# Kernel optimization log

Measured on AMD Instinct MI355X. Metric: run time of the kernel, lower is better.

The kernel has to match this reference:

```python
import jax, jax.numpy as jnp
import numpy as np

NUM_LEVELS = 3
NUM_EMBEDDINGS = 1024
EMBEDDING_DIM = 128
COMMITMENT_COST = 0.25
N_TOKENS = 262144


def setup_inputs() -> dict:
    key = jax.random.key(0)
    k1, k2 = jax.random.split(key)
    z_e = jax.random.normal(k1, (N_TOKENS, EMBEDDING_DIM), dtype=jnp.float32)
    codebooks = jax.random.normal(k2, (NUM_LEVELS, NUM_EMBEDDINGS, EMBEDDING_DIM), dtype=jnp.float32)
    return {"z_e": z_e, "codebooks": codebooks}


def _rvq_forward(z_e, codebooks):
    """Sequential residual VQ: per level cdist + argmin + gather + residual update.

    Per-level losses follow the standard EMA-VQ formulation:
      vq_loss     = mean((z_q - sg(residual))^2)
      commit_loss = beta * mean((sg(z_q) - residual)^2)
    with straight-through estimator z_q_st = residual + sg(z_q - residual).
    """
    sg = jax.lax.stop_gradient
    residual = z_e
    z_q_total = jnp.zeros_like(z_e)
    all_indices = []
    vq_loss = jnp.float32(0.0)
    commit_loss = jnp.float32(0.0)
    num_levels = codebooks.shape[0]
    for lvl in range(num_levels):  # small fixed loop over levels (sequential by design)
        E = codebooks[lvl]  # [K, D]
        # squared-distance matrix [N, K]: ||r||^2 + ||e||^2 - 2 r.e
        d = (jnp.sum(residual * residual, axis=1, keepdims=True)
             + jnp.sum(E * E, axis=1)
             - 2.0 * (residual @ E.T))
        idx = jnp.argmin(d, axis=1)           # [N]
        z_q = E[idx]                           # gather [N, D]
        vq_loss = vq_loss + jnp.mean((z_q - sg(residual)) ** 2)
        commit_loss = commit_loss + COMMITMENT_COST * jnp.mean((sg(z_q) - residual) ** 2)
        z_q_st = residual + sg(z_q - residual)  # straight-through
        z_q_total = z_q_total + z_q_st
        residual = residual - z_q_st
        all_indices.append(idx)
    L = jnp.float32(num_levels)
    stacked_indices = jnp.stack(all_indices, axis=1)  # [N, num_levels]
    return z_q_total, vq_loss / L, commit_loss / L, stacked_indices


def reference(z_e, codebooks):
    return _rvq_forward(z_e, codebooks)
```

## Files before the change

kernel.cpp:

```cpp
#include <hip/hip_runtime.h>
#include <math.h>

#define N_TOK   262144
#define DIMV    128
#define KCODE   1024
#define LEV     3
#define BLOCK   256
#define NTILES  64
#define EPS     0.08f

typedef _Float16 f16x8 __attribute__((ext_vector_type(8)));
typedef float f32x4 __attribute__((ext_vector_type(4)));


__global__ void rvq_prep(const float* __restrict__ cb, double* __restrict__ ws) {
    int c = blockIdx.x * blockDim.x + threadIdx.x;
    if (c == 0) ws[0] = 0.0;
    if (c < LEV * KCODE) {
        const float* e = cb + (size_t)c * DIMV;
        double s = 0.0;
        #pragma unroll 8
        for (int j = 0; j < DIMV; ++j) { double v = (double)e[j]; s = fma(v, v, s); }
        ws[8 + c] = s;
        ((float*)(ws + 8 + LEV * KCODE))[c] = (float)(s + 8192.0);
    }
}

__device__ inline void stage_write(unsigned char* dst, int woff, float4 g0, float4 g1) {
    f16x8 v;
    v[0]=(_Float16)g0.x; v[1]=(_Float16)g0.y; v[2]=(_Float16)g0.z; v[3]=(_Float16)g0.w;
    v[4]=(_Float16)g1.x; v[5]=(_Float16)g1.y; v[6]=(_Float16)g1.z; v[7]=(_Float16)g1.w;
    *(f16x8*)(dst + woff) = v;
}

__device__ inline unsigned sel4(const unsigned v[4], int j) {
    unsigned a = (j & 1) ? v[1] : v[0];
    unsigned b = (j & 1) ? v[3] : v[2];
    return (j & 2) ? b : a;
}

__global__ __launch_bounds__(BLOCK, 2) void rvq_main(const float* __restrict__ ze,
                                                     const float* __restrict__ cb,
                                                     float* __restrict__ out,
                                                     double* __restrict__ ws) {
    __shared__ __align__(16) unsigned char Bbuf[8][4096];
    __shared__ __align__(16) float eeS[KCODE];
    __shared__ double ssum[4];

    const double* __restrict__ ee64g = ws + 8;
    const float*  __restrict__ eebg  = (const float*)(ws + 8 + LEV * KCODE);

    const int tid  = threadIdx.x;
    const int lane = tid & 63;
    const int wid  = tid >> 6;
    const int q    = lane >> 4;
    const int col  = lane & 15;
    const long tokbase = (long)blockIdx.x * 128 + wid * 32;

    const int wc   = (((tid >> 2) & 3) << 6) | ((tid & 3) << 4) | (tid >> 4);
    const int woff = (wc ^ ((wc >> 4) & 7)) << 4;
    const int ro_e = (lane ^ (lane >> 4)) << 4;
    const int ro_o = (lane ^ 4 ^ (lane >> 4)) << 4;

    float r[2][4][8];
    f16x8 Ah[2][4], Al[2][4];

    #pragma unroll
    for (int mt = 0; mt < 2; ++mt) {
        const float4* zp = (const float4*)(ze + (size_t)(tokbase + mt*16 + col) * DIMV);
        #pragma unroll
        for (int st = 0; st < 4; ++st) {
            float4 a = zp[st*8 + q*2], b = zp[st*8 + q*2 + 1];
            r[mt][st][0]=a.x; r[mt][st][1]=a.y; r[mt][st][2]=a.z; r[mt][st][3]=a.w;
            r[mt][st][4]=b.x; r[mt][st][5]=b.y; r[mt][st][6]=b.z; r[mt][st][7]=b.w;
        }
    }
    #pragma unroll
    for (int mt = 0; mt < 2; ++mt)
        #pragma unroll
        for (int st = 0; st < 4; ++st) {
            f16x8 h, lo;
            #pragma unroll
            for (int j = 0; j < 8; ++j) {
                float y = -2.0f * r[mt][st][j];
                _Float16 hh = (_Float16)y;
                h[j] = hh;
                lo[j] = (_Float16)(y - (float)hh);
            }
            Ah[mt][st] = h; Al[mt][st] = lo;
        }

    double loss = 0.0;
    float* out_idx = out + (size_t)N_TOK * DIMV + 2;

    for (int l = 0; l < LEV; ++l) {
        __syncthreads();
        ((float4*)eeS)[tid] = ((const float4*)(eebg + (size_t)l * KCODE))[tid];
        {
            const float4* p = (const float4*)(cb + ((size_t)l*KCODE + (tid>>4)) * DIMV + (tid&15)*8);
            #pragma unroll
            for (int i = 0; i < 4; ++i) {
                stage_write(Bbuf[i], woff, p[0], p[1]);
                p += 512;
            }
        }
        __syncthreads();

        const float4* pp = (const float4*)(cb + ((size_t)l*KCODE + 64 + (tid>>4)) * DIMV + (tid&15)*8);

        unsigned m1[2][4], m2[2][4];
        #pragma unroll
        for (int mt = 0; mt < 2; ++mt)
            #pragma unroll
            for (int i = 0; i < 4; ++i) { m1[mt][i] = 0xFFFFFFFFu; m2[mt][i] = 0xFFFFFFFFu; }

        for (int tb = 0; tb < NTILES; tb += 4) {
            const int pre = (tb + 4 < NTILES);
            #pragma unroll
            for (int s = 0; s < 4; ++s) {
                const int t = tb + s;
                float4 g0, g1;
                if (pre) { g0 = pp[0]; g1 = pp[1]; pp += 512; }
                {
                    const unsigned char* bb = Bbuf[t & 7];
                    f16x8 B0 = *(const f16x8*)(bb + ro_e);
                    f16x8 B1 = *(const f16x8*)(bb + 1024 + ro_o);
                    f16x8 B2 = *(const f16x8*)(bb + 2048 + ro_e);
                    f16x8 B3 = *(const f16x8*)(bb + 3072 + ro_o);
                    float eeq = eeS[t*16 + col];
                    f32x4 c0  = {eeq, eeq, eeq, eeq};
                    f32x4 c1v = {eeq, eeq, eeq, eeq};
                    c0  = __builtin_amdgcn_mfma_f32_16x16x32_f16(Ah[0][0], B0, c0, 0,0,0);
                    c1v = __builtin_amdgcn_mfma_f32_16x16x32_f16(Ah[1][0], B0, c1v, 0,0,0);
                    c0  = __builtin_amdgcn_mfma_f32_16x16x32_f16(Al[0][0], B0, c0, 0,0,0);
                    c1v = __builtin_amdgcn_mfma_f32_16x16x32_f16(Al[1][0], B0, c1v, 0,0,0);
                    c0  = __builtin_amdgcn_mfma_f32_16x16x32_f16(Ah[0][1], B1, c0, 0,0,0);
                    c1v = __builtin_amdgcn_mfma_f32_16x16x32_f16(Ah[1][1], B1, c1v, 0,0,0);
                    c0  = __builtin_amdgcn_mfma_f32_16x16x32_f16(Al[0][1], B1, c0, 0,0,0);
                    c1v = __builtin_amdgcn_mfma_f32_16x16x32_f16(Al[1][1], B1, c1v, 0,0,0);
                    c0  = __builtin_amdgcn_mfma_f32_16x16x32_f16(Ah[0][2], B2, c0, 0,0,0);
                    c1v = __builtin_amdgcn_mfma_f32_16x16x32_f16(Ah[1][2], B2, c1v, 0,0,0);
                    c0  = __builtin_amdgcn_mfma_f32_16x16x32_f16(Al[0][2], B2, c0, 0,0,0);
                    c1v = __builtin_amdgcn_mfma_f32_16x16x32_f16(Al[1][2], B2, c1v, 0,0,0);
                    c0  = __builtin_amdgcn_mfma_f32_16x16x32_f16(Ah[0][3], B3, c0, 0,0,0);
                    c1v = __builtin_amdgcn_mfma_f32_16x16x32_f16(Ah[1][3], B3, c1v, 0,0,0);
                    c0  = __builtin_amdgcn_mfma_f32_16x16x32_f16(Al[0][3], B3, c0, 0,0,0);
                    c1v = __builtin_amdgcn_mfma_f32_16x16x32_f16(Al[1][3], B3, c1v, 0,0,0);
                    #pragma unroll
                    for (int i = 0; i < 4; ++i) {
                        unsigned k0 = (__float_as_uint(c0[i]) << 6) | (unsigned)t;
                        m2[0][i] = min(m2[0][i], max(m1[0][i], k0));
                        m1[0][i] = min(m1[0][i], k0);
                        unsigned k1_ = (__float_as_uint(c1v[i]) << 6) | (unsigned)t;
                        m2[1][i] = min(m2[1][i], max(m1[1][i], k1_));
                        m1[1][i] = min(m1[1][i], k1_);
                    }
                }
                if (pre) stage_write(Bbuf[(t+4)&7], woff, g0, g1);
            }
            __syncthreads();
        }

        unsigned k1[2][4], k2[2][4], q1[2][4], q2[2][4];
        #pragma unroll
        for (int mt = 0; mt < 2; ++mt)
            #pragma unroll
            for (int i = 0; i < 4; ++i) {
                k1[mt][i] = m1[mt][i]; k2[mt][i] = m2[mt][i];
                q1[mt][i] = (unsigned)col; q2[mt][i] = (unsigned)col;
            }
        #pragma unroll
        for (int d = 1; d <= 8; d <<= 1) {
            #pragma unroll
            for (int mt = 0; mt < 2; ++mt)
                #pragma unroll
                for (int i = 0; i < 4; ++i) {
                    unsigned ok1 = __shfl_xor(k1[mt][i], d), oq1 = __shfl_xor(q1[mt][i], d);
                    unsigned ok2 = __shfl_xor(k2[mt][i], d), oq2 = __shfl_xor(q2[mt][i], d);
                    bool sw = (ok1 < k1[mt][i]) || (ok1 == k1[mt][i] && oq1 < q1[mt][i]);
                    unsigned n1 = sw ? ok1 : k1[mt][i], nq1 = sw ? oq1 : q1[mt][i];
                    unsigned hk = sw ? k1[mt][i] : ok1, hq = sw ? q1[mt][i] : oq1;
                    bool s2 = (ok2 < k2[mt][i]) || (ok2 == k2[mt][i] && oq2 < q2[mt][i]);
                    unsigned p2 = s2 ? ok2 : k2[mt][i], pq = s2 ? oq2 : q2[mt][i];
                    bool s3 = (p2 < hk) || (p2 == hk && pq < hq);
                    k1[mt][i] = n1;              q1[mt][i] = nq1;
                    k2[mt][i] = s3 ? p2 : hk;    q2[mt][i] = s3 ? pq : hq;
                }
        }

        int jsel = (lane >> 2) & 3;
        int S = ((col >> 2) << 4) | ((col & 3) << 2);

        #pragma unroll
        for (int mt = 0; mt < 2; ++mt) {
            unsigned sk1 = sel4(k1[mt], jsel), sq1 = sel4(q1[mt], jsel);
            unsigned sk2 = sel4(k2[mt], jsel), sq2 = sel4(q2[mt], jsel);
            unsigned bk1 = (unsigned)__shfl((int)sk1, S);
            unsigned bq1 = (unsigned)__shfl((int)sq1, S);
            unsigned bk2 = (unsigned)__shfl((int)sk2, S);
            unsigned bq2 = (unsigned)__shfl((int)sq2, S);
            int c1c = (int)(((bk1 & 63u) << 4) | bq1);
            int c2c = (int)(((bk2 & 63u) << 4) | bq2);
            float d1 = __uint_as_float((bk1 >> 6) | 0x44000000u) - 8192.0f;
            float d2 = __uint_as_float((bk2 >> 6) | 0x44000000u) - 8192.0f;
            int bc = c1c;
            if (d2 - d1 < EPS) {
                double s1 = 0.0, s2d = 0.0;
                const float4* e1 = (const float4*)(cb + ((size_t)l*KCODE + c1c)*DIMV);
                const float4* e2 = (const float4*)(cb + ((size_t)l*KCODE + c2c)*DIMV);
                #pragma unroll
                for (int st = 0; st < 4; ++st) {
                    float4 a = e1[st*8 + q*2], b = e1[st*8 + q*2 + 1];
                    s1 = fma((double)a.x,(double)r[mt][st][0],s1); s1 = fma((double)a.y,(double)r[mt][st][1],s1);
                    s1 = fma((double)a.z,(double)r[mt][st][2],s1); s1 = fma((double)a.w,(double)r[mt][st][3],s1);
                    s1 = fma((double)b.x,(double)r[mt][st][4],s1); s1 = fma((double)b.y,(double)r[mt][st][5],s1);
                    s1 = fma((double)b.z,(double)r[mt][st][6],s1); s1 = fma((double)b.w,(double)r[mt][st][7],s1);
                    float4 a2 = e2[st*8 + q*2], b2 = e2[st*8 + q*2 + 1];
                    s2d = fma((double)a2.x,(double)r[mt][st][0],s2d); s2d = fma((double)a2.y,(double)r[mt][st][1],s2d);
                    s2d = fma((double)a2.z,(double)r[mt][st][2],s2d); s2d = fma((double)a2.w,(double)r[mt][st][3],s2d);
                    s2d = fma((double)b2.x,(double)r[mt][st][4],s2d); s2d = fma((double)b2.y,(double)r[mt][st][5],s2d);
                    s2d = fma((double)b2.z,(double)r[mt][st][6],s2d); s2d = fma((double)b2.w,(double)r[mt][st][7],s2d);
                }
                s1  += __shfl_xor(s1, 16);  s1  += __shfl_xor(s1, 32);
                s2d += __shfl_xor(s2d, 16); s2d += __shfl_xor(s2d, 32);
                double dd1 = ee64g[l*KCODE + c1c] - 2.0*s1;
                double dd2 = ee64g[l*KCODE + c2c] - 2.0*s2d;
                if (dd2 < dd1 || (dd2 == dd1 && c2c < c1c)) bc = c2c;
            }
            const float4* eb = (const float4*)(cb + ((size_t)l*KCODE + bc)*DIMV);
            #pragma unroll
            for (int st = 0; st < 4; ++st) {
                float4 a = eb[st*8 + q*2], b = eb[st*8 + q*2 + 1];
                float qv[8] = {a.x,a.y,a.z,a.w,b.x,b.y,b.z,b.w};
                #pragma unroll
                for (int j = 0; j < 8; ++j) {
                    float rv = r[mt][st][j];
                    float t1 = qv[j] - rv;
                    loss += (double)t1 * (double)t1;
                    float zqst = rv + t1;
                    r[mt][st][j] = rv - zqst;
                }
            }
            if (l < LEV - 1) {
                #pragma unroll
                for (int st = 0; st < 4; ++st) {
                    f16x8 h, lo;
                    #pragma unroll
                    for (int j = 0; j < 8; ++j) {
                        float y = -2.0f * r[mt][st][j];
                        _Float16 hh = (_Float16)y;
                        h[j] = hh;
                        lo[j] = (_Float16)(y - (float)hh);
                    }
                    Ah[mt][st] = h; Al[mt][st] = lo;
                }
            } else {
                const float4* zp = (const float4*)(ze + (size_t)(tokbase + mt*16 + col)*DIMV);
                float4* op = (float4*)(out + (size_t)(tokbase + mt*16 + col)*DIMV);
                #pragma unroll
                for (int st = 0; st < 4; ++st) {
                    float4 za = zp[st*8 + q*2], zb = zp[st*8 + q*2 + 1];
                    float4 oa, ob;
                    oa.x = za.x - r[mt][st][0]; oa.y = za.y - r[mt][st][1];
                    oa.z = za.z - r[mt][st][2]; oa.w = za.w - r[mt][st][3];
                    ob.x = zb.x - r[mt][st][4]; ob.y = zb.y - r[mt][st][5];
                    ob.z = zb.z - r[mt][st][6]; ob.w = zb.w - r[mt][st][7];
                    op[st*8 + q*2] = oa; op[st*8 + q*2 + 1] = ob;
                }
            }
            if (q == 0) out_idx[(size_t)(tokbase + mt*16 + col)*3 + l] = (float)bc;
        }
    }

    #pragma unroll
    for (int d = 1; d <= 32; d <<= 1) loss += __shfl_xor(loss, d);
    if ((tid & 63) == 0) ssum[wid] = loss;
    __syncthreads();
    if (tid == 0) atomicAdd(ws, ssum[0] + ssum[1] + ssum[2] + ssum[3]);
}

__global__ void rvq_fin(const double* __restrict__ ws, float* __restrict__ out) {
    double vq = ws[0] / ((double)N_TOK * (double)DIMV * (double)LEV);
    out[(size_t)N_TOK * DIMV + 0] = (float)vq;
    out[(size_t)N_TOK * DIMV + 1] = (float)(0.25 * vq);
}

extern "C" void kernel_launch(void* const* d_in, const int* in_sizes, int n_in,
                              void* d_out, int out_size, void* d_ws, size_t ws_size,
                              hipStream_t stream) {
    const float* ze = (const float*)d_in[0];
    const float* cb = (const float*)d_in[1];
    float* out = (float*)d_out;
    double* ws = (double*)d_ws;

    rvq_prep<<<(LEV * KCODE + 255) / 256, 256, 0, stream>>>(cb, ws);
    rvq_main<<<N_TOK / 128, BLOCK, 0, stream>>>(ze, cb, out, ws);
    rvq_fin<<<1, 1, 0, stream>>>(ws, out);
}
```

Baseline: 708.4 us.

## Prepack codebook into MFMA fragment layout and stream B operands from global

The prep kernel now converts each codebook to fp16 and writes it in the exact per-lane MFMA B-fragment layout in the workspace, alongside the norms. The main kernel drops shared-memory staging, the fp32-to-fp16 conversion and per-tile __syncthreads. Each wave instead loads its B fragments straight from global/L2 with a two-tile register double buffer. This removes LDS traffic and barriers but makes every wave read the codebook separately from cache, so the loop is more exposed to global load latency.

```diff
diff --git a/kernel.cpp b/kernel.cpp
--- a/kernel.cpp
+++ b/kernel.cpp
@@ -9,28 +9,38 @@
 #define NTILES  64
 #define EPS     0.08f
 
+#define WS_EE64_B  64
+#define WS_EE32_B  24640
+#define WS_FRAG_B  36928
+
 typedef _Float16 f16x8 __attribute__((ext_vector_type(8)));
 typedef float f32x4 __attribute__((ext_vector_type(4)));
-
 
 __global__ void rvq_prep(const float* __restrict__ cb, double* __restrict__ ws) {
     int c = blockIdx.x * blockDim.x + threadIdx.x;
     if (c == 0) ws[0] = 0.0;
-    if (c < LEV * KCODE) {
-        const float* e = cb + (size_t)c * DIMV;
-        double s = 0.0;
-        #pragma unroll 8
-        for (int j = 0; j < DIMV; ++j) { double v = (double)e[j]; s = fma(v, v, s); }
-        ws[8 + c] = s;
-        ((float*)(ws + 8 + LEV * KCODE))[c] = (float)(s + 8192.0);
-    }
-}
-
-__device__ inline void stage_write(unsigned char* dst, int woff, float4 g0, float4 g1) {
-    f16x8 v;
-    v[0]=(_Float16)g0.x; v[1]=(_Float16)g0.y; v[2]=(_Float16)g0.z; v[3]=(_Float16)g0.w;
-    v[4]=(_Float16)g1.x; v[5]=(_Float16)g1.y; v[6]=(_Float16)g1.z; v[7]=(_Float16)g1.w;
-    *(f16x8*)(dst + woff) = v;
+    if (c >= LEV * KCODE) return;
+    const float* e = cb + (size_t)c * DIMV;
+    const int lvl = c >> 10, ci = c & 1023, t4 = ci >> 4, n = ci & 15;
+    unsigned char* fb = (unsigned char*)ws + WS_FRAG_B + (((size_t)(lvl * 64 + t4)) << 12);
+    double s = 0.0;
+    #pragma unroll
+    for (int st = 0; st < 4; ++st)
+        #pragma unroll
+        for (int kq = 0; kq < 4; ++kq) {
+            float4 a = *(const float4*)(e + st*32 + kq*8);
+            float4 b = *(const float4*)(e + st*32 + kq*8 + 4);
+            f16x8 h;
+            h[0]=(_Float16)a.x; h[1]=(_Float16)a.y; h[2]=(_Float16)a.z; h[3]=(_Float16)a.w;
+            h[4]=(_Float16)b.x; h[5]=(_Float16)b.y; h[6]=(_Float16)b.z; h[7]=(_Float16)b.w;
+            s = fma((double)a.x,(double)a.x,s); s = fma((double)a.y,(double)a.y,s);
+            s = fma((double)a.z,(double)a.z,s); s = fma((double)a.w,(double)a.w,s);
+            s = fma((double)b.x,(double)b.x,s); s = fma((double)b.y,(double)b.y,s);
+            s = fma((double)b.z,(double)b.z,s); s = fma((double)b.w,(double)b.w,s);
+            *(f16x8*)(fb + st*1024 + ((kq*16 + n) << 4)) = h;
+        }
+    ((double*)((unsigned char*)ws + WS_EE64_B))[c] = s;
+    ((float*)((unsigned char*)ws + WS_EE32_B))[c] = (float)(s + 8192.0);
 }
 
 __device__ inline unsigned sel4(const unsigned v[4], int j) {
@@ -43,12 +53,11 @@
                                                      const float* __restrict__ cb,
                                                      float* __restrict__ out,
                                                      double* __restrict__ ws) {
-    __shared__ __align__(16) unsigned char Bbuf[8][4096];
-    __shared__ __align__(16) float eeS[KCODE];
     __shared__ double ssum[4];
 
-    const double* __restrict__ ee64g = ws + 8;
-    const float*  __restrict__ eebg  = (const float*)(ws + 8 + LEV * KCODE);
+    const double* __restrict__ ee64g = (const double*)((const unsigned char*)ws + WS_EE64_B);
+    const float*  __restrict__ eebg  = (const float*)((const unsigned char*)ws + WS_EE32_B);
+    const unsigned char* __restrict__ fbase = (const unsigned char*)ws + WS_FRAG_B;
 
     const int tid  = threadIdx.x;
     const int lane = tid & 63;
@@ -57,11 +66,6 @@
     const int col  = lane & 15;
     const long tokbase = (long)blockIdx.x * 128 + wid * 32;
 
-    const int wc   = (((tid >> 2) & 3) << 6) | ((tid & 3) << 4) | (tid >> 4);
-    const int woff = (wc ^ ((wc >> 4) & 7)) << 4;
-    const int ro_e = (lane ^ (lane >> 4)) << 4;
-    const int ro_o = (lane ^ 4 ^ (lane >> 4)) << 4;
-
     float r[2][4][8];
     f16x8 Ah[2][4], Al[2][4];
 
@@ -93,20 +97,45 @@
     double loss = 0.0;
     float* out_idx = out + (size_t)N_TOK * DIMV + 2;
 
+#define TILE_COMPUTE(B, EEQ, T)                                                      \
+    do {                                                                             \
+        f32x4 c0  = {(EEQ),(EEQ),(EEQ),(EEQ)};                                       \
+        f32x4 c1v = {(EEQ),(EEQ),(EEQ),(EEQ)};                                       \
+        c0  = __builtin_amdgcn_mfma_f32_16x16x32_f16(Ah[0][0], (B)[0], c0,  0,0,0);  \
+        c1v = __builtin_amdgcn_mfma_f32_16x16x32_f16(Ah[1][0], (B)[0], c1v, 0,0,0);  \
+        c0  = __builtin_amdgcn_mfma_f32_16x16x32_f16(Al[0][0], (B)[0], c0,  0,0,0);  \
+        c1v = __builtin_amdgcn_mfma_f32_16x16x32_f16(Al[1][0], (B)[0], c1v, 0,0,0);  \
+        c0  = __builtin_amdgcn_mfma_f32_16x16x32_f16(Ah[0][1], (B)[1], c0,  0,0,0);  \
+        c1v = __builtin_amdgcn_mfma_f32_16x16x32_f16(Ah[1][1], (B)[1], c1v, 0,0,0);  \
+        c0  = __builtin_amdgcn_mfma_f32_16x16x32_f16(Al[0][1], (B)[1], c0,  0,0,0);  \
+        c1v = __builtin_amdgcn_mfma_f32_16x16x32_f16(Al[1][1], (B)[1], c1v, 0,0,0);  \
+        c0  = __builtin_amdgcn_mfma_f32_16x16x32_f16(Ah[0][2], (B)[2], c0,  0,0,0);  \
+        c1v = __builtin_amdgcn_mfma_f32_16x16x32_f16(Ah[1][2], (B)[2], c1v, 0,0,0);  \
+        c0  = __builtin_amdgcn_mfma_f32_16x16x32_f16(Al[0][2], (B)[2], c0,  0,0,0);  \
+        c1v = __builtin_amdgcn_mfma_f32_16x16x32_f16(Al[1][2], (B)[2], c1v, 0,0,0);  \
+        c0  = __builtin_amdgcn_mfma_f32_16x16x32_f16(Ah[0][3], (B)[3], c0,  0,0,0);  \
+        c1v = __builtin_amdgcn_mfma_f32_16x16x32_f16(Ah[1][3], (B)[3], c1v, 0,0,0);  \
+        c0  = __builtin_amdgcn_mfma_f32_16x16x32_f16(Al[0][3], (B)[3], c0,  0,0,0);  \
+        c1v = __builtin_amdgcn_mfma_f32_16x16x32_f16(Al[1][3], (B)[3], c1v, 0,0,0);  \
+        _Pragma("unroll")                                                            \
+        for (int i = 0; i < 4; ++i) {                                                \
+            unsigned k0 = (__float_as_uint(c0[i]) << 6) | (unsigned)(T);             \
+            m2[0][i] = min(m2[0][i], max(m1[0][i], k0));                             \
+            m1[0][i] = min(m1[0][i], k0);                                            \
+            unsigned k1_ = (__float_as_uint(c1v[i]) << 6) | (unsigned)(T);           \
+            m2[1][i] = min(m2[1][i], max(m1[1][i], k1_));                            \
+            m1[1][i] = min(m1[1][i], k1_);                                           \
+        }                                                                            \
+    } while (0)
+
     for (int l = 0; l < LEV; ++l) {
-        __syncthreads();
-        ((float4*)eeS)[tid] = ((const float4*)(eebg + (size_t)l * KCODE))[tid];
-        {
-            const float4* p = (const float4*)(cb + ((size_t)l*KCODE + (tid>>4)) * DIMV + (tid&15)*8);
-            #pragma unroll
-            for (int i = 0; i < 4; ++i) {
-                stage_write(Bbuf[i], woff, p[0], p[1]);
-                p += 512;
-            }
-        }
-        __syncthreads();
-
-        const float4* pp = (const float4*)(cb + ((size_t)l*KCODE + 64 + (tid>>4)) * DIMV + (tid&15)*8);
+        const unsigned char* bp = fbase + ((size_t)l << 18) + (lane << 4);
+        const float* eep = eebg + l * KCODE + col;
+
+        f16x8 Ba[4], Bb[4];
+        #pragma unroll
+        for (int st = 0; st < 4; ++st) Ba[st] = *(const f16x8*)(bp + st*1024);
+        float eeq_a = eep[0], eeq_b;
 
         unsigned m1[2][4], m2[2][4];
         #pragma unroll
@@ -114,51 +143,23 @@
             #pragma unroll
             for (int i = 0; i < 4; ++i) { m1[mt][i] = 0xFFFFFFFFu; m2[mt][i] = 0xFFFFFFFFu; }
 
-        for (int tb = 0; tb < NTILES; tb += 4) {
-            const int pre = (tb + 4 < NTILES);
-            #pragma unroll
-            for (int s = 0; s < 4; ++s) {
-                const int t = tb + s;
-                float4 g0, g1;
-                if (pre) { g0 = pp[0]; g1 = pp[1]; pp += 512; }
-                {
-                    const unsigned char* bb = Bbuf[t & 7];
-                    f16x8 B0 = *(const f16x8*)(bb + ro_e);
-                    f16x8 B1 = *(const f16x8*)(bb + 1024 + ro_o);
-                    f16x8 B2 = *(const f16x8*)(bb + 2048 + ro_e);
-                    f16x8 B3 = *(const f16x8*)(bb + 3072 + ro_o);
-                    float eeq = eeS[t*16 + col];
-                    f32x4 c0  = {eeq, eeq, eeq, eeq};
-                    f32x4 c1v = {eeq, eeq, eeq, eeq};
-                    c0  = __builtin_amdgcn_mfma_f32_16x16x32_f16(Ah[0][0], B0, c0, 0,0,0);
-                    c1v = __builtin_amdgcn_mfma_f32_16x16x32_f16(Ah[1][0], B0, c1v, 0,0,0);
-                    c0  = __builtin_amdgcn_mfma_f32_16x16x32_f16(Al[0][0], B0, c0, 0,0,0);
-                    c1v = __builtin_amdgcn_mfma_f32_16x16x32_f16(Al[1][0], B0, c1v, 0,0,0);
-                    c0  = __builtin_amdgcn_mfma_f32_16x16x32_f16(Ah[0][1], B1, c0, 0,0,0);
-                    c1v = __builtin_amdgcn_mfma_f32_16x16x32_f16(Ah[1][1], B1, c1v, 0,0,0);
-                    c0  = __builtin_amdgcn_mfma_f32_16x16x32_f16(Al[0][1], B1, c0, 0,0,0);
-                    c1v = __builtin_amdgcn_mfma_f32_16x16x32_f16(Al[1][1], B1, c1v, 0,0,0);
-                    c0  = __builtin_amdgcn_mfma_f32_16x16x32_f16(Ah[0][2], B2, c0, 0,0,0);
-                    c1v = __builtin_amdgcn_mfma_f32_16x16x32_f16(Ah[1][2], B2, c1v, 0,0,0);
-                    c0  = __builtin_amdgcn_mfma_f32_16x16x32_f16(Al[0][2], B2, c0, 0,0,0);
-                    c1v = __builtin_amdgcn_mfma_f32_16x16x32_f16(Al[1][2], B2, c1v, 0,0,0);
-                    c0  = __builtin_amdgcn_mfma_f32_16x16x32_f16(Ah[0][3], B3, c0, 0,0,0);
-                    c1v = __builtin_amdgcn_mfma_f32_16x16x32_f16(Ah[1][3], B3, c1v, 0,0,0);
-                    c0  = __builtin_amdgcn_mfma_f32_16x16x32_f16(Al[0][3], B3, c0, 0,0,0);
-                    c1v = __builtin_amdgcn_mfma_f32_16x16x32_f16(Al[1][3], B3, c1v, 0,0,0);
-                    #pragma unroll
-                    for (int i = 0; i < 4; ++i) {
-                        unsigned k0 = (__float_as_uint(c0[i]) << 6) | (unsigned)t;
-                        m2[0][i] = min(m2[0][i], max(m1[0][i], k0));
-                        m1[0][i] = min(m1[0][i], k0);
-                        unsigned k1_ = (__float_as_uint(c1v[i]) << 6) | (unsigned)t;
-                        m2[1][i] = min(m2[1][i], max(m1[1][i], k1_));
-                        m1[1][i] = min(m1[1][i], k1_);
-                    }
-                }
-                if (pre) stage_write(Bbuf[(t+4)&7], woff, g0, g1);
-            }
-            __syncthreads();
+        for (int t = 0; t < NTILES; t += 2) {
+            {
+                const unsigned char* np = bp + 4096;
+                #pragma unroll
+                for (int st = 0; st < 4; ++st) Bb[st] = *(const f16x8*)(np + st*1024);
+                eeq_b = eep[16];
+            }
+            TILE_COMPUTE(Ba, eeq_a, t);
+            {
+                const unsigned char* np = (t + 2 < NTILES) ? bp + 8192 : bp;
+                const float* ep2 = (t + 2 < NTILES) ? eep + 32 : eep;
+                #pragma unroll
+                for (int st = 0; st < 4; ++st) Ba[st] = *(const f16x8*)(np + st*1024);
+                eeq_a = ep2[0];
+            }
+            TILE_COMPUTE(Bb, eeq_b, t + 1);
+            bp += 8192; eep += 32;
         }
 
         unsigned k1[2][4], k2[2][4], q1[2][4], q2[2][4];
```

Result: slower. 733.9 us (+3.6%).
